# Kernel optimization log

Measured on AMD Instinct MI355X. Metric: run time of the kernel, lower is better.

Reference implementation:

```python
import jax, jax.numpy as jnp
import numpy as np

VOCAB = 32000
DIM = 128
BATCH = 1024
CONTEXT = 10


def setup_inputs() -> dict:
    key = jax.random.key(0)
    k_idx, k_emb, k_out = jax.random.split(key, 3)
    # context word indices -> one-hot batch [B, C, V], as the original feeds a dense one-hot tensor
    idx = jax.random.randint(k_idx, (BATCH, CONTEXT), 0, VOCAB)
    batch = jax.nn.one_hot(idx, VOCAB, dtype=jnp.float32)
    emb = jax.random.normal(k_emb, (VOCAB, DIM), dtype=jnp.float32)
    w_out = jax.random.normal(k_out, (DIM, VOCAB), dtype=jnp.float32)
    return {"batch": batch, "emb": emb, "w_out": w_out}


def reference(batch, emb, w_out):
    # embedding lookup expressed as one-hot matmul, exactly as the original
    embedding = jnp.einsum('bcv,vd->bcd', batch, emb)      # [B, C, D]
    avg_embedding = jnp.mean(embedding, axis=1)            # [B, D]
    linear_output = avg_embedding @ w_out                  # [B, V]
    return jax.nn.softmax(linear_output, axis=-1)
```

## Files before the change

kernel.cpp:

```cpp
#include <hip/hip_runtime.h>
#include <hip/hip_bf16.h>

#define VOCAB 32000
#define DIM   128
#define BATCH 1024
#define CTX   10
#define SHIFT 20.0f

typedef __bf16 bf16x8 __attribute__((ext_vector_type(8)));
typedef float  f32x4  __attribute__((ext_vector_type(4)));

static __device__ __forceinline__ unsigned short bf16_hi(float x) {
    __hip_bfloat16 h = __float2bfloat16(x);
    return __builtin_bit_cast(unsigned short, h);
}
static __device__ __forceinline__ float bf16_back(unsigned short u) {
    __hip_bfloat16 h = __builtin_bit_cast(__hip_bfloat16, u);
    return __bfloat162float(h);
}

__global__ __launch_bounds__(256) void convert_w_kernel(
    const float* __restrict__ w, unsigned short* __restrict__ wth,
    unsigned short* __restrict__ wtl) {
    const int n  = blockIdx.x * 256 + threadIdx.x;
    const int k0 = blockIdx.y * 32;
    for (int k = k0; k < k0 + 32; ++k) {
        float x = w[k * VOCAB + n];
        unsigned short h = bf16_hi(x);
        unsigned short l = bf16_hi(x - bf16_back(h));
        wth[n * DIM + k] = h;
        wtl[n * DIM + k] = l;
    }
}

__global__ __launch_bounds__(256) void onehot_idx_kernel(
    const float* __restrict__ batch, int* __restrict__ idx) {
    const unsigned int total4 = (unsigned int)BATCH * CTX * (VOCAB / 4);
    const unsigned int S = gridDim.x * blockDim.x;
    const uint4* __restrict__ b4 = reinterpret_cast<const uint4*>(batch);
    unsigned int i = blockIdx.x * blockDim.x + threadIdx.x;

    auto emit = [&](uint4 v, unsigned int ii) {
        if ((v.x | v.y | v.z | v.w) != 0u) {
            unsigned int e   = ii * 4u;
            unsigned int row = e / VOCAB;
            unsigned int col = e - row * VOCAB;
            if      (v.x) idx[row] = (int)col;
            else if (v.y) idx[row] = (int)col + 1;
            else if (v.z) idx[row] = (int)col + 2;
            else          idx[row] = (int)col + 3;
        }
    };

    for (; i + S < total4; i += 2 * S) {
        uint4 v0 = b4[i];
        uint4 v1 = b4[i + S];
        emit(v0, i);
        emit(v1, i + S);
    }
    if (i < total4) emit(b4[i], i);
}

__global__ __launch_bounds__(128) void avg_emb_kernel(
    const int* __restrict__ idx, const float* __restrict__ emb,
    unsigned short* __restrict__ avgh, unsigned short* __restrict__ avgl) {
    int b = blockIdx.x;
    int d = threadIdx.x;
    float s = 0.f;
#pragma unroll
    for (int c = 0; c < CTX; ++c) {
        int id = idx[b * CTX + c];
        s += emb[id * DIM + d];
    }
    s *= (1.f / CTX);
    unsigned short h = bf16_hi(s);
    unsigned short l = bf16_hi(s - bf16_back(h));
    avgh[b * DIM + d] = h;
    avgl[b * DIM + d] = l;
}

__global__ __launch_bounds__(256) void gemm_exp_kernel(
    const unsigned short* __restrict__ ah, const unsigned short* __restrict__ al,
    const unsigned short* __restrict__ wth, const unsigned short* __restrict__ wtl,
    float* __restrict__ out) {
    const int tid  = threadIdx.x;
    const int wv   = tid >> 6;
    const int lane = tid & 63;
    const int l15  = lane & 15;
    const int kg   = lane >> 4;

    const int m0 = blockIdx.y * 64 + wv * 16;
    const int n0 = blockIdx.x * 64;

    const unsigned short* pah = ah  + (m0 + l15) * DIM + kg * 8;
    const unsigned short* pal = al  + (m0 + l15) * DIM + kg * 8;
    const unsigned short* pbh = wth + (n0 + l15) * DIM + kg * 8;
    const unsigned short* pbl = wtl + (n0 + l15) * DIM + kg * 8;

    f32x4 acc[4] = {{0.f,0.f,0.f,0.f},{0.f,0.f,0.f,0.f},
                    {0.f,0.f,0.f,0.f},{0.f,0.f,0.f,0.f}};

#pragma unroll
    for (int k0 = 0; k0 < DIM; k0 += 32) {
        bf16x8 a_h = *reinterpret_cast<const bf16x8*>(pah + k0);
        bf16x8 a_l = *reinterpret_cast<const bf16x8*>(pal + k0);
#pragma unroll
        for (int nt = 0; nt < 4; ++nt) {
            bf16x8 b_h = *reinterpret_cast<const bf16x8*>(pbh + nt * 16 * DIM + k0);
            bf16x8 b_l = *reinterpret_cast<const bf16x8*>(pbl + nt * 16 * DIM + k0);
            acc[nt] = __builtin_amdgcn_mfma_f32_16x16x32_bf16(a_h, b_h, acc[nt], 0, 0, 0);
            acc[nt] = __builtin_amdgcn_mfma_f32_16x16x32_bf16(a_h, b_l, acc[nt], 0, 0, 0);
            acc[nt] = __builtin_amdgcn_mfma_f32_16x16x32_bf16(a_l, b_h, acc[nt], 0, 0, 0);
        }
    }

#pragma unroll
    for (int nt = 0; nt < 4; ++nt) {
        const int col = n0 + nt * 16 + l15;
#pragma unroll
        for (int r = 0; r < 4; ++r) {
            const int row = m0 + kg * 4 + r;
            out[(long long)row * VOCAB + col] = __expf(acc[nt][r] - SHIFT);
        }
    }
}

__global__ __launch_bounds__(512) void sumscale_kernel(float* __restrict__ out) {
    float4* p = reinterpret_cast<float4*>(out + (long long)blockIdx.x * VOCAB);
    const int tid  = threadIdx.x;
    const int lane = tid & 63;
    const int wave = tid >> 6;
    __shared__ float red[8];

    const int N4 = VOCAB / 4;
    float s = 0.f;
    int i = tid;
    for (; i + 512 < N4; i += 1024) {
        float4 a = p[i];
        float4 b = p[i + 512];
        s += ((a.x + a.y) + (a.z + a.w)) + ((b.x + b.y) + (b.z + b.w));
    }
    if (i < N4) {
        float4 a = p[i];
        s += (a.x + a.y) + (a.z + a.w);
    }
#pragma unroll
    for (int d = 1; d < 64; d <<= 1) s += __shfl_xor(s, d, 64);
    if (lane == 0) red[wave] = s;
    __syncthreads();
    const float inv = 1.f / (((red[0] + red[1]) + (red[2] + red[3])) +
                             ((red[4] + red[5]) + (red[6] + red[7])));

    for (int k = tid; k < N4; k += 512) {
        float4 v = p[k];
        v.x *= inv; v.y *= inv; v.z *= inv; v.w *= inv;
        p[k] = v;
    }
}

extern "C" void kernel_launch(void* const* d_in, const int* in_sizes, int n_in,
                              void* d_out, int out_size, void* d_ws, size_t ws_size,
                              hipStream_t stream) {
    const float* batch = (const float*)d_in[0];
    const float* emb   = (const float*)d_in[1];
    const float* w_out = (const float*)d_in[2];
    float*       out   = (float*)d_out;

    char* ws = (char*)d_ws;
    int*            idx  = (int*)ws;            ws += BATCH * CTX * sizeof(int);
    unsigned short* avgh = (unsigned short*)ws; ws += BATCH * DIM * sizeof(short);
    unsigned short* avgl = (unsigned short*)ws; ws += BATCH * DIM * sizeof(short);
    unsigned short* wth  = (unsigned short*)ws; ws += (size_t)VOCAB * DIM * sizeof(short);
    unsigned short* wtl  = (unsigned short*)ws;

    convert_w_kernel<<<dim3(VOCAB / 256, 4), 256, 0, stream>>>(w_out, wth, wtl);
    onehot_idx_kernel<<<2048, 256, 0, stream>>>(batch, idx);
    avg_emb_kernel<<<BATCH, DIM, 0, stream>>>(idx, emb, avgh, avgl);
    gemm_exp_kernel<<<dim3(VOCAB / 64, BATCH / 64), 256, 0, stream>>>(avgh, avgl, wth, wtl, out);
    sumscale_kernel<<<BATCH, 512, 0, stream>>>(out);
}
```

Baseline: 499.3 us.

## Fuse softmax row sums into GEMM epilogue and swizzle operands for MFMA

The row-sum reduction moves into the GEMM epilogue, using shuffle reductions and atomicAdd into a per-row partial-sum buffer that is zeroed in the index kernel. The separate read pass over the output in the normalize kernel goes away, leaving a single scale pass. The weight and activation bf16 splits are written in an MFMA-fragment-swizzled layout so each lane does one coalesced 16-byte load, and each GEMM block now covers 128 rows to reuse B fragments. The cost is float atomics, which make the summation order nondeterministic, plus extra shared-memory staging in the embedding kernel.

```diff
diff --git a/kernel.cpp b/kernel.cpp
--- a/kernel.cpp
+++ b/kernel.cpp
@@ -19,26 +19,38 @@
     return __bfloat162float(h);
 }
 
+
+union u4s8 { uint4 v; unsigned short s[8]; };
+
 __global__ __launch_bounds__(256) void convert_w_kernel(
-    const float* __restrict__ w, unsigned short* __restrict__ wth,
-    unsigned short* __restrict__ wtl) {
-    const int n  = blockIdx.x * 256 + threadIdx.x;
-    const int k0 = blockIdx.y * 32;
-    for (int k = k0; k < k0 + 32; ++k) {
-        float x = w[k * VOCAB + n];
-        unsigned short h = bf16_hi(x);
-        unsigned short l = bf16_hi(x - bf16_back(h));
-        wth[n * DIM + k] = h;
-        wtl[n * DIM + k] = l;
+    const float* __restrict__ w, uint4* __restrict__ wsh, uint4* __restrict__ wsl) {
+    const int n   = blockIdx.x * 256 + threadIdx.x;
+    const int k0i = blockIdx.y;
+    const int base = (n >> 4) * 256 + k0i * 64 + (n & 15);
+#pragma unroll
+    for (int kg = 0; kg < 4; ++kg) {
+        u4s8 vh, vl;
+#pragma unroll
+        for (int j = 0; j < 8; ++j) {
+            float x = w[(k0i * 32 + kg * 8 + j) * VOCAB + n];
+            unsigned short hh = bf16_hi(x);
+            vh.s[j] = hh;
+            vl.s[j] = bf16_hi(x - bf16_back(hh));
+        }
+        wsh[base + kg * 16] = vh.v;
+        wsl[base + kg * 16] = vl.v;
     }
 }
 
 __global__ __launch_bounds__(256) void onehot_idx_kernel(
-    const float* __restrict__ batch, int* __restrict__ idx) {
+    const float* __restrict__ batch, int* __restrict__ idx,
+    float* __restrict__ psum) {
+    const unsigned int g = blockIdx.x * blockDim.x + threadIdx.x;
+    if (g < BATCH) psum[g] = 0.f;
+
     const unsigned int total4 = (unsigned int)BATCH * CTX * (VOCAB / 4);
     const unsigned int S = gridDim.x * blockDim.x;
     const uint4* __restrict__ b4 = reinterpret_cast<const uint4*>(batch);
-    unsigned int i = blockIdx.x * blockDim.x + threadIdx.x;
 
     auto emit = [&](uint4 v, unsigned int ii) {
         if ((v.x | v.y | v.z | v.w) != 0u) {
@@ -52,6 +64,7 @@
         }
     };
 
+    unsigned int i = g;
     for (; i + S < total4; i += 2 * S) {
         uint4 v0 = b4[i];
         uint4 v1 = b4[i + S];
@@ -63,9 +76,10 @@
 
 __global__ __launch_bounds__(128) void avg_emb_kernel(
     const int* __restrict__ idx, const float* __restrict__ emb,
-    unsigned short* __restrict__ avgh, unsigned short* __restrict__ avgl) {
-    int b = blockIdx.x;
-    int d = threadIdx.x;
+    uint4* __restrict__ ash, uint4* __restrict__ asl) {
+    __shared__ unsigned short sh[DIM], sl[DIM];
+    const int b = blockIdx.x;
+    const int d = threadIdx.x;
     float s = 0.f;
 #pragma unroll
     for (int c = 0; c < CTX; ++c) {
@@ -73,85 +87,90 @@
         s += emb[id * DIM + d];
     }
     s *= (1.f / CTX);
-    unsigned short h = bf16_hi(s);
-    unsigned short l = bf16_hi(s - bf16_back(h));
-    avgh[b * DIM + d] = h;
-    avgl[b * DIM + d] = l;
+    unsigned short hh = bf16_hi(s);
+    sh[d] = hh;
+    sl[d] = bf16_hi(s - bf16_back(hh));
+    __syncthreads();
+    if (d < 16) {
+        u4s8 vh, vl;
+#pragma unroll
+        for (int j = 0; j < 8; ++j) { vh.s[j] = sh[d * 8 + j]; vl.s[j] = sl[d * 8 + j]; }
+        const int pos = (b >> 4) * 256 + d * 16 + (b & 15);
+        ash[pos] = vh.v;
+        asl[pos] = vl.v;
+    }
 }
 
 __global__ __launch_bounds__(256) void gemm_exp_kernel(
-    const unsigned short* __restrict__ ah, const unsigned short* __restrict__ al,
-    const unsigned short* __restrict__ wth, const unsigned short* __restrict__ wtl,
-    float* __restrict__ out) {
+    const uint4* __restrict__ ash, const uint4* __restrict__ asl,
+    const uint4* __restrict__ wsh, const uint4* __restrict__ wsl,
+    float* __restrict__ out, float* __restrict__ psum) {
     const int tid  = threadIdx.x;
     const int wv   = tid >> 6;
     const int lane = tid & 63;
     const int l15  = lane & 15;
     const int kg   = lane >> 4;
 
-    const int m0 = blockIdx.y * 64 + wv * 16;
-    const int n0 = blockIdx.x * 64;
-
-    const unsigned short* pah = ah  + (m0 + l15) * DIM + kg * 8;
-    const unsigned short* pal = al  + (m0 + l15) * DIM + kg * 8;
-    const unsigned short* pbh = wth + (n0 + l15) * DIM + kg * 8;
-    const unsigned short* pbl = wtl + (n0 + l15) * DIM + kg * 8;
-
-    f32x4 acc[4] = {{0.f,0.f,0.f,0.f},{0.f,0.f,0.f,0.f},
-                    {0.f,0.f,0.f,0.f},{0.f,0.f,0.f,0.f}};
-
-#pragma unroll
-    for (int k0 = 0; k0 < DIM; k0 += 32) {
-        bf16x8 a_h = *reinterpret_cast<const bf16x8*>(pah + k0);
-        bf16x8 a_l = *reinterpret_cast<const bf16x8*>(pal + k0);
+    const int m_b0 = blockIdx.y * 128 + wv * 16;
+    const int n0   = blockIdx.x * 64;
+
+    f32x4 acc[2][4] = {};
+
+#pragma unroll
+    for (int k0i = 0; k0i < 4; ++k0i) {
+        bf16x8 a_h[2], a_l[2], b_h[4], b_l[4];
+#pragma unroll
+        for (int mt = 0; mt < 2; ++mt) {
+            const int ai = ((m_b0 + mt * 64) >> 4) * 256 + k0i * 64 + lane;
+            a_h[mt] = *reinterpret_cast<const bf16x8*>(ash + ai);
+            a_l[mt] = *reinterpret_cast<const bf16x8*>(asl + ai);
+        }
 #pragma unroll
         for (int nt = 0; nt < 4; ++nt) {
-            bf16x8 b_h = *reinterpret_cast<const bf16x8*>(pbh + nt * 16 * DIM + k0);
-            bf16x8 b_l = *reinterpret_cast<const bf16x8*>(pbl + nt * 16 * DIM + k0);
-            acc[nt] = __builtin_amdgcn_mfma_f32_16x16x32_bf16(a_h, b_h, acc[nt], 0, 0, 0);
-            acc[nt] = __builtin_amdgcn_mfma_f32_16x16x32_bf16(a_h, b_l, acc[nt], 0, 0, 0);
-            acc[nt] = __builtin_amdgcn_mfma_f32_16x16x32_bf16(a_l, b_h, acc[nt], 0, 0, 0);
-        }
-    }
-
-#pragma unroll
-    for (int nt = 0; nt < 4; ++nt) {
-        const int col = n0 + nt * 16 + l15;
+            const int bi = ((n0 >> 4) + nt) * 256 + k0i * 64 + lane;
+            b_h[nt] = *reinterpret_cast<const bf16x8*>(wsh + bi);
+            b_l[nt] = *reinterpret_cast<const bf16x8*>(wsl + bi);
+        }
+#pragma unroll
+        for (int mt = 0; mt < 2; ++mt)
+#pragma unroll
+            for (int nt = 0; nt < 4; ++nt) {
+                acc[mt][nt] = __builtin_amdgcn_mfma_f32_16x16x32_bf16(a_h[mt], b_h[nt], acc[mt][nt], 0, 0, 0);
+                acc[mt][nt] = __builtin_amdgcn_mfma_f32_16x16x32_bf16(a_h[mt], b_l[nt], acc[mt][nt], 0, 0, 0);
+                acc[mt][nt] = __builtin_amdgcn_mfma_f32_16x16x32_bf16(a_l[mt], b_h[nt], acc[mt][nt], 0, 0, 0);
+            }
+    }
+
+#pragma unroll
+    for (int mt = 0; mt < 2; ++mt) {
+        float rs[4] = {0.f, 0.f, 0.f, 0.f};
+#pragma unroll
+        for (int nt = 0; nt < 4; ++nt) {
+            const int col = n0 + nt * 16 + l15;
+#pragma unroll
+            for (int r = 0; r < 4; ++r) {
+                const int row = m_b0 + mt * 64 + kg * 4 + r;
+                float e = __expf(acc[mt][nt][r] - SHIFT);
+                out[(long long)row * VOCAB + col] = e;
+                rs[r] += e;
+            }
+        }
 #pragma unroll
         for (int r = 0; r < 4; ++r) {
-            const int row = m0 + kg * 4 + r;
-            out[(long long)row * VOCAB + col] = __expf(acc[nt][r] - SHIFT);
-        }
-    }
-}
-
-__global__ __launch_bounds__(512) void sumscale_kernel(float* __restrict__ out) {
+#pragma unroll
+            for (int dd = 1; dd < 16; dd <<= 1)
+                rs[r] += __shfl_xor(rs[r], dd, 64);
+            if (l15 == 0)
+                atomicAdd(&psum[m_b0 + mt * 64 + kg * 4 + r], rs[r]);
+        }
+    }
+}
+
+__global__ __launch_bounds__(512) void finalize_kernel(
+    const float* __restrict__ psum, float* __restrict__ out) {
+    const float inv = 1.f / psum[blockIdx.x];
     float4* p = reinterpret_cast<float4*>(out + (long long)blockIdx.x * VOCAB);
-    const int tid  = threadIdx.x;
-    const int lane = tid & 63;
-    const int wave = tid >> 6;
-    __shared__ float red[8];
-
-    const int N4 = VOCAB / 4;
-    float s = 0.f;
-    int i = tid;
-    for (; i + 512 < N4; i += 1024) {
-        float4 a = p[i];
-        float4 b = p[i + 512];
-        s += ((a.x + a.y) + (a.z + a.w)) + ((b.x + b.y) + (b.z + b.w));
-    }
-    if (i < N4) {
-        float4 a = p[i];
-        s += (a.x + a.y) + (a.z + a.w);
-    }
-#pragma unroll
-    for (int d = 1; d < 64; d <<= 1) s += __shfl_xor(s, d, 64);
-    if (lane == 0) red[wave] = s;
-    __syncthreads();
-    const float inv = 1.f / (((red[0] + red[1]) + (red[2] + red[3])) +
-                             ((red[4] + red[5]) + (red[6] + red[7])));
-
-    for (int k = tid; k < N4; k += 512) {
+    for (int k = threadIdx.x; k < VOCAB / 4; k += 512) {
         float4 v = p[k];
         v.x *= inv; v.y *= inv; v.z *= inv; v.w *= inv;
         p[k] = v;
@@ -167,15 +186,17 @@
     float*       out   = (float*)d_out;
 
     char* ws = (char*)d_ws;
-    int*            idx  = (int*)ws;            ws += BATCH * CTX * sizeof(int);
-    unsigned short* avgh = (unsigned short*)ws; ws += BATCH * DIM * sizeof(short);
-    unsigned short* avgl = (unsigned short*)ws; ws += BATCH * DIM * sizeof(short);
-    unsigned short* wth  = (unsigned short*)ws; ws += (size_t)VOCAB * DIM * sizeof(short);
-    unsigned short* wtl  = (unsigned short*)ws;
-
-    convert_w_kernel<<<dim3(VOCAB / 256, 4), 256, 0, stream>>>(w_out, wth, wtl);
-    onehot_idx_kernel<<<2048, 256, 0, stream>>>(batch, idx);
-    avg_emb_kernel<<<BATCH, DIM, 0, stream>>>(idx, emb, avgh, avgl);
-    gemm_exp_kernel<<<dim3(VOCAB / 64, BATCH / 64), 256, 0, stream>>>(avgh, avgl, wth, wtl, out);
-    sumscale_kernel<<<BATCH, 512, 0, stream>>>(out);
-}
+    int*   idx  = (int*)ws;   ws += BATCH * CTX * sizeof(int);
+    float* psum = (float*)ws; ws += BATCH * sizeof(float);
+    ws = (char*)(((size_t)ws + 255) & ~(size_t)255);
+    uint4* ash  = (uint4*)ws; ws += (size_t)(BATCH / 16) * 256 * 16;
+    uint4* asl  = (uint4*)ws; ws += (size_t)(BATCH / 16) * 256 * 16;
+    uint4* wsh  = (uint4*)ws; ws += (size_t)(VOCAB / 16) * 256 * 16;
+    uint4* wsl  = (uint4*)ws;
+
+    convert_w_kernel<<<dim3(VOCAB / 256, 4), 256, 0, stream>>>(w_out, wsh, wsl);
+    onehot_idx_kernel<<<2048, 256, 0, stream>>>(batch, idx, psum);
+    avg_emb_kernel<<<BATCH, DIM, 0, stream>>>(idx, emb, ash, asl);
+    gemm_exp_kernel<<<dim3(VOCAB / 64, BATCH / 128), 256, 0, stream>>>(ash, asl, wsh, wsl, out, psum);
+    finalize_kernel<<<BATCH, 512, 0, stream>>>(psum, out);
+}
```

New measurement: 468.7 us. -6.1%, faster.
